# Performance work log

Measured on AMD Instinct MI355X. Metric: run time of the kernel, lower is better.

The kernel has to match this reference:

```python
import jax, jax.numpy as jnp
import numpy as np


def _lrelu(x):
    return jnp.where(x >= 0, x, 0.2 * x)


def _mod_conv(x, style, w_mod, weight, stride, demodulate):
    # x: (B, Cin, H, W); style: (B, S); w_mod: (Cin, S); weight: (Cout, Cin, k, k)
    B, Cin, H, W = x.shape
    Cout, _, k, _ = weight.shape
    scale = 1.0 / np.sqrt(Cin * k * k)
    s = style @ w_mod.T                                   # (B, Cin) per-sample modulation
    w = scale * weight[None] * s[:, None, :, None, None]  # (B, Cout, Cin, k, k)
    if demodulate:
        d = jax.lax.rsqrt(jnp.sum(w * w, axis=(2, 3, 4)) + 1e-8)
        w = w * d[:, :, None, None, None]
    w = w.reshape(B * Cout, Cin, k, k)
    xr = x.reshape(1, B * Cin, H, W)
    pad = k // 2
    out = jax.lax.conv_general_dilated(
        xr, w, (stride, stride), [(pad, pad), (pad, pad)],
        dimension_numbers=('NCHW', 'OIHW', 'NCHW'), feature_group_count=B)
    return out.reshape(B, Cout, out.shape[2], out.shape[3])


def _mapping(z, labels, emb, map_W, map_b, map_g, map_beta):
    x = z + emb[labels]
    for i in range(map_W.shape[0]):
        x = x @ map_W[i].T + map_b[i]
        mu = jnp.mean(x, axis=0)
        var = jnp.var(x, axis=0)  # biased, as torch BatchNorm uses for normalization
        x = (x - mu) * jax.lax.rsqrt(var + 1e-5) * map_g[i] + map_beta[i]
        x = _lrelu(x)
    return x


def _block(x, w, c1w, c1m, c2w, c2m, n1w, n2w, na, nb):
    x = _mod_conv(x, w, c1m, c1w, 1, True)
    x = _lrelu(x + n1w[None, :, None, None] * na)
    x = _mod_conv(x, w, c2m, c2w, 2, True)  # up=2 -> stride=2 strided conv (as in source)
    x = _lrelu(x + n2w[None, :, None, None] * nb)
    return x


def setup_inputs() -> dict:
    key = jax.random.key(0)
    ks = iter(jax.random.split(key, 64))
    nrm = lambda shape, s=1.0: jax.random.normal(next(ks), shape, jnp.float32) * s
    B, Z, Wd, L, LAB = 8, 512, 512, 8, 10
    inp = {}
    inp['z'] = nrm((B, Z))
    inp['labels'] = jax.random.randint(next(ks), (B,), 0, LAB)
    inp['emb'] = nrm((LAB, Z), 0.1)
    inp['map_W'] = nrm((L, Wd, Z), float(np.sqrt(2.0 / Z)))
    inp['map_b'] = jnp.zeros((L, Wd), jnp.float32)
    inp['map_g'] = jnp.ones((L, Wd), jnp.float32)
    inp['map_beta'] = jnp.zeros((L, Wd), jnp.float32)
    inp['const'] = nrm((128, 256, 256))
    inp['b1c1_w'] = nrm((128, 128, 3, 3)); inp['b1c1_m'] = nrm((128, Wd), 0.04)
    inp['b1c2_w'] = nrm((128, 128, 3, 3)); inp['b1c2_m'] = nrm((128, Wd), 0.04)
    inp['b1n1_w'] = nrm((128,), 0.1); inp['b1n2_w'] = nrm((128,), 0.1)
    inp['b2c1_w'] = nrm((64, 128, 3, 3)); inp['b2c1_m'] = nrm((128, Wd), 0.04)
    inp['b2c2_w'] = nrm((64, 64, 3, 3)); inp['b2c2_m'] = nrm((64, Wd), 0.04)
    inp['b2n1_w'] = nrm((64,), 0.1); inp['b2n2_w'] = nrm((64,), 0.1)
    inp['b3c1_w'] = nrm((32, 64, 3, 3)); inp['b3c1_m'] = nrm((64, Wd), 0.04)
    inp['b3c2_w'] = nrm((32, 32, 3, 3)); inp['b3c2_m'] = nrm((32, Wd), 0.04)
    inp['b3n1_w'] = nrm((32,), 0.1); inp['b3n2_w'] = nrm((32,), 0.1)
    inp['rgb_w'] = nrm((1, 32, 1, 1)); inp['rgb_m'] = nrm((32, Wd), 0.04)
    inp['n1a'] = nrm((B, 1, 256, 256)); inp['n1b'] = nrm((B, 1, 128, 128))
    inp['n2a'] = nrm((B, 1, 128, 128)); inp['n2b'] = nrm((B, 1, 64, 64))
    inp['n3a'] = nrm((B, 1, 64, 64)); inp['n3b'] = nrm((B, 1, 32, 32))
    return inp


def reference(z, labels, emb, map_W, map_b, map_g, map_beta, const,
              b1c1_w, b1c1_m, b1c2_w, b1c2_m, b1n1_w, b1n2_w,
              b2c1_w, b2c1_m, b2c2_w, b2c2_m, b2n1_w, b2n2_w,
              b3c1_w, b3c1_m, b3c2_w, b3c2_m, b3n1_w, b3n2_w,
              rgb_w, rgb_m, n1a, n1b, n2a, n2b, n3a, n3b):
    B = z.shape[0]
    w = _mapping(z, labels, emb, map_W, map_b, map_g, map_beta)
    x = jnp.broadcast_to(const[None], (B,) + const.shape)
    x = _block(x, w, b1c1_w, b1c1_m, b1c2_w, b1c2_m, b1n1_w, b1n2_w, n1a, n1b)
    x = _block(x, w, b2c1_w, b2c1_m, b2c2_w, b2c2_m, b2n1_w, b2n2_w, n2a, n2b)
    x = _block(x, w, b3c1_w, b3c1_m, b3c2_w, b3c2_m, b3n1_w, b3n2_w, n3a, n3b)
    # final block: F.interpolate(..., size=(256,240), mode='bilinear', align_corners=False)
    x = jax.image.resize(x, (B, x.shape[1], 256, 240), method='bilinear')
    out = _mod_conv(x, w, rgb_m, rgb_w, 1, False)  # to-grayscale 1x1, no demod
    return out
```

## Files before the change

kernel.cpp:

```cpp
#include <hip/hip_runtime.h>
#include <hip/hip_bf16.h>


typedef __hip_bfloat16 bf16;
typedef __attribute__((ext_vector_type(8))) short bf16x8;
typedef __attribute__((ext_vector_type(4))) float f32x4;

__device__ __forceinline__ float b2f(bf16 v){ return __bfloat162float(v); }
__device__ __forceinline__ bf16  f2b(float v){ return __float2bfloat16(v); }
__device__ __forceinline__ unsigned short bbits(float v){
  bf16 h = f2b(v); union { bf16 h; unsigned short u; } x; x.h = h; return x.u;
}
__device__ __forceinline__ float ldf(const void* p, size_t i, int isf32){
  return isf32 ? ((const float*)p)[i] : b2f(((const bf16*)p)[i]);
}
__device__ __forceinline__ void stf(void* p, size_t i, int isf32, float v){
  if (isf32) ((float*)p)[i] = v; else ((bf16*)p)[i] = f2b(v);
}

__global__ __launch_bounds__(256) void detect_dtype(const unsigned short* __restrict__ cst,
    int* __restrict__ flag){
  __shared__ int cnt[256];
  int t = threadIdx.x, c = 0;
  for (int i=t; i<4096; i+=256){
    unsigned short w = cst[i];
    int mag = w & 0x7FFF;
    int e = mag >> 7;
    if (mag == 0 || (e >= 96 && e <= 150)) c++;
  }
  cnt[t] = c; __syncthreads();
  for (int s=128; s>0; s>>=1){ if (t<s) cnt[t] += cnt[t+s]; __syncthreads(); }
  if (t == 0) *flag = (cnt[0] >= 3500) ? 0 : 1;
}

__global__ __launch_bounds__(256) void cvt_const(const void* __restrict__ cst,
    short* __restrict__ out, const int* __restrict__ dflag){
  int isf32 = *dflag;
  __shared__ __align__(16) short sh[64*136];
  int t = threadIdx.x;
  int p0 = blockIdx.x * 64;
  for (int i=t; i<128*64; i+=256){
    int ci = i >> 6, px = i & 63;
    float v = ldf(cst, (size_t)ci*65536 + p0 + px, isf32);
    sh[px*136 + ci] = (short)bbits(v);
  }
  __syncthreads();
  for (int i=t; i<64*16; i+=256){
    int px = i >> 4, c8 = (i & 15) * 8;
    bf16x8 val = *(const bf16x8*)&sh[px*136 + c8];
    *(bf16x8*)(out + ((size_t)(p0+px))*128 + c8) = val;
  }
}

__global__ __launch_bounds__(256) void map_init(const void* __restrict__ z,
    const int* __restrict__ labels, const void* __restrict__ emb,
    float* __restrict__ x0, const int* __restrict__ dflag){
  int isf32 = *dflag;
  int i = blockIdx.x*256 + threadIdx.x;
  int b = i >> 9, k = i & 511;
  x0[i] = ldf(z, i, isf32) + ldf(emb, (size_t)labels[b]*512 + k, isf32);
}

__global__ __launch_bounds__(64) void map_layer(const float* __restrict__ xin,
    float* __restrict__ xout, const void* __restrict__ W, size_t wOff,
    const void* __restrict__ bl, const void* __restrict__ gl,
    const void* __restrict__ betal, size_t vOff, const int* __restrict__ dflag){
  int isf32 = *dflag;
  int j = blockIdx.x;
  int l = threadIdx.x;
  int b = l >> 3, sp = l & 7;
  float part = 0.f;
  int k0 = sp*64;
  size_t wrow = wOff + (size_t)j*512 + k0;
  for (int k=0; k<64; k++)
    part += xin[b*512 + k0 + k] * ldf(W, wrow + k, isf32);
  part += __shfl_xor(part, 1);
  part += __shfl_xor(part, 2);
  part += __shfl_xor(part, 4);
  float y = part + ldf(bl, vOff + j, isf32);
  float ys[8];
  float mu = 0.f;
  #pragma unroll
  for (int bb=0; bb<8; bb++){ ys[bb] = __shfl(y, bb*8); mu += ys[bb]; }
  mu *= 0.125f;
  float var = 0.f;
  #pragma unroll
  for (int bb=0; bb<8; bb++){ float d = ys[bb]-mu; var += d*d; }
  var *= 0.125f;
  float xn = (y-mu)*rsqrtf(var+1e-5f)*ldf(gl, vOff + j, isf32) + ldf(betal, vOff + j, isf32);
  xn = (xn >= 0.f) ? xn : 0.2f*xn;
  if (sp == 0) xout[b*512 + j] = xn;
}

__global__ __launch_bounds__(64) void styles_kernel(const float* __restrict__ w,
    float* __restrict__ s_all,
    const void* m0, const void* m1, const void* m2, const void* m3,
    const void* m4, const void* m5, const void* m6, const int* __restrict__ dflag){
  int isf32 = *dflag;
  int id = blockIdx.x;
  const int offs[8] = {0,1024,2048,3072,3584,4096,4352,4608};
  const int cins[7] = {128,128,128,64,64,32,32};
  const void* ms[7] = {m0,m1,m2,m3,m4,m5,m6};
  int c = 0;
  while (id >= offs[c+1]) c++;
  int r = id - offs[c];
  int Cin = cins[c];
  int b = r / Cin, ci = r % Cin;
  int l = threadIdx.x;
  float acc = 0.f;
  for (int k=l; k<512; k+=64) acc += w[b*512 + k] * ldf(ms[c], (size_t)ci*512 + k, isf32);
  #pragma unroll
  for (int m=1; m<64; m<<=1) acc += __shfl_xor(acc, m);
  if (l == 0) s_all[id] = acc;
}

__global__ __launch_bounds__(64) void modw_kernel(const float* __restrict__ s_all,
    bf16* __restrict__ wmod,
    const void* w0, const void* w1, const void* w2, const void* w3,
    const void* w4, const void* w5, const void* w6, const int* __restrict__ dflag){
  int isf32 = *dflag;
  int bid = blockIdx.x;
  int base, Cout, Cin, soff, wmoff, demod = 1;
  const void* wp;
  if      (bid < 1024){ base=0;    Cout=128; Cin=128; soff=0;    wmoff=0;       wp=w0; }
  else if (bid < 2048){ base=1024; Cout=128; Cin=128; soff=1024; wmoff=1179648; wp=w1; }
  else if (bid < 2560){ base=2048; Cout=64;  Cin=128; soff=2048; wmoff=2359296; wp=w2; }
  else if (bid < 3072){ base=2560; Cout=64;  Cin=64;  soff=3072; wmoff=2949120; wp=w3; }
  else if (bid < 3328){ base=3072; Cout=32;  Cin=64;  soff=3584; wmoff=3244032; wp=w4; }
  else if (bid < 3584){ base=3328; Cout=32;  Cin=32;  soff=4096; wmoff=3391488; wp=w5; }
  else                { base=3584; Cout=1;   Cin=32;  soff=4352; wmoff=3465216; wp=w6; demod=0; }
  int kk = demod ? 9 : 1;
  int L  = Cin * kk;
  int bc = bid - base;
  int b  = bc / Cout, co = bc % Cout;
  float scale = 1.0f / sqrtf((float)L);
  int l = threadIdx.x;
  float part = 0.f;
  for (int e=l; e<L; e+=64){
    int ci = e / kk;
    float v = scale * ldf(wp, (size_t)co*L + e, isf32) * s_all[soff + b*Cin + ci];
    part += v*v;
  }
  #pragma unroll
  for (int m=1; m<64; m<<=1) part += __shfl_xor(part, m);
  float d = demod ? rsqrtf(part + 1e-8f) : 1.0f;
  for (int e=l; e<L; e+=64){
    int ci = e / kk, tap = e % kk;
    float v = scale * ldf(wp, (size_t)co*L + e, isf32) * s_all[soff + b*Cin + ci];
    size_t idx;
    if (demod){
      int c32 = ci >> 5;
      int lane2 = ((ci >> 3) & 3) * 16 + (co & 15);
      int j = ci & 7;
      int mtg = co >> 4;
      idx = (size_t)wmoff +
            ((((size_t)b*9 + tap)*(Cin>>5) + c32)*(Cout>>4) + mtg)*512 + lane2*8 + j;
    } else {
      idx = (size_t)wmoff + (size_t)b*Cin + e;
    }
    wmod[idx] = f2b(v * d);
  }
}

template<int MT, int NT, int S, int WT, int NR>
__global__ __launch_bounds__(256, 4) void convmf(
    const short* __restrict__ X, long long xbs, int Cin, int Hin, int Win,
    const bf16* __restrict__ WA, const void* __restrict__ noise,
    const void* __restrict__ nwp, short* __restrict__ Y, long long ybs,
    int Cout, int Hout, int Wout, const int* __restrict__ dflag){
  constexpr int W_in_t = (S==1) ? (WT+2) : (2*WT+1);
  constexpr int R_in   = (S==1) ? (NR+2) : (2*NR+1);
  constexpr int ENT    = R_in * W_in_t;
  __shared__ __align__(16) short act[ENT*40];
  int isf32 = *dflag;
  int t = threadIdx.x;
  int lane = t & 63, wv = t >> 6;
  int mw = wv & 1, nwv = wv >> 1;
  int lanelow = lane & 15, quad = lane >> 4;
  int tiles_x = Wout / WT;
  int tx = blockIdx.x % tiles_x, ty = blockIdx.x / tiles_x;
  int ox0 = tx*WT, oy0 = ty*NR;
  int iy0 = S*oy0 - 1, ix0 = S*ox0 - 1;
  int z = blockIdx.z;
  const short* Xb = X + (size_t)z * xbs;
  short* Yb = Y + (size_t)z * ybs;
  const int Cin32 = Cin >> 5, Cout16 = Cout >> 4;
  const bf16x8* WAimg = (const bf16x8*)WA + (size_t)z * 9 * Cin32 * Cout16 * 64;
  f32x4 acc[MT][NT];
  #pragma unroll
  for (int mt=0; mt<MT; mt++)
    #pragma unroll
    for (int nt=0; nt<NT; nt++) acc[mt][nt] = (f32x4){0.f,0.f,0.f,0.f};
  int rowb[NT], xb[NT];
  #pragma unroll
  for (int nt=0; nt<NT; nt++){
    int nl = nwv*NT*16 + nt*16;
    rowb[nt] = nl / WT;
    xb[nt]  = nl % WT + lanelow;
  }
  for (int c32=0; c32<Cin32; c32++){
    int c0 = c32 << 5;
    __syncthreads();
    for (int i=t; i<ENT; i+=256){
      int r = i / W_in_t, x = i - r*W_in_t;
      int gy = iy0 + r, gx = ix0 + x;
      bf16x8* dst = (bf16x8*)&act[i*40];
      if (gy>=0 && gy<Hin && gx>=0 && gx<Win){
        const bf16x8* src = (const bf16x8*)(Xb + ((size_t)gy*Win + gx)*Cin + c0);
        dst[0]=src[0]; dst[1]=src[1]; dst[2]=src[2]; dst[3]=src[3];
      } else {
        bf16x8 zz = (bf16x8){0,0,0,0,0,0,0,0};
        dst[0]=zz; dst[1]=zz; dst[2]=zz; dst[3]=zz;
      }
    }
    __syncthreads();
    #pragma unroll
    for (int tap=0; tap<9; tap++){
      int ky = tap/3, kx = tap%3;
      bf16x8 afr[MT], bfr[NT];
      #pragma unroll
      for (int mt=0; mt<MT; mt++){
        int mtg = mw*MT + mt;
        afr[mt] = WAimg[(((size_t)tap*Cin32 + c32)*Cout16 + mtg)*64 + lane];
      }
      #pragma unroll
      for (int nt=0; nt<NT; nt++){
        int off = ((S*rowb[nt] + ky)*W_in_t + (S*xb[nt] + kx))*40 + quad*8;
        bfr[nt] = *(const bf16x8*)&act[off];
      }
      #pragma unroll
      for (int mt=0; mt<MT; mt++)
        #pragma unroll
        for (int nt=0; nt<NT; nt++)
          acc[mt][nt] = __builtin_amdgcn_mfma_f32_16x16x32_bf16(
              afr[mt], bfr[nt], acc[mt][nt], 0, 0, 0);
    }
  }
  #pragma unroll
  for (int nt=0; nt<NT; nt++){
    int oy = oy0 + rowb[nt], ox = ox0 + xb[nt];
    float nv = ldf(noise, ((size_t)z*Hout + oy)*Wout + ox, isf32);
    #pragma unroll
    for (int mt=0; mt<MT; mt++){
      int co0 = (mw*MT + mt)*16 + quad*4;
      ushort4 pk;
      float v0 = acc[mt][nt][0] + ldf(nwp, co0+0, isf32)*nv; v0 = (v0>=0.f)?v0:0.2f*v0;
      float v1 = acc[mt][nt][1] + ldf(nwp, co0+1, isf32)*nv; v1 = (v1>=0.f)?v1:0.2f*v1;
      float v2 = acc[mt][nt][2] + ldf(nwp, co0+2, isf32)*nv; v2 = (v2>=0.f)?v2:0.2f*v2;
      float v3 = acc[mt][nt][3] + ldf(nwp, co0+3, isf32)*nv; v3 = (v3>=0.f)?v3:0.2f*v3;
      pk.x = bbits(v0); pk.y = bbits(v1); pk.z = bbits(v2); pk.w = bbits(v3);
      *(ushort4*)&Yb[((size_t)oy*Wout + ox)*Cout + co0] = pk;
    }
  }
}

__global__ __launch_bounds__(256) void resize_rgb(const short* __restrict__ X,
    long long xbs, const bf16* __restrict__ wr, void* __restrict__ out,
    const int* __restrict__ dflag){
  int isf32 = *dflag;
  int b = blockIdx.y;
  const short* Xb = X + (size_t)b * xbs;
  int i = blockIdx.x*256 + threadIdx.x;
  int x = i % 240;
  int y = i / 240;
  float sy = (y + 0.5f)*0.125f - 0.5f;
  float sx = (x + 0.5f)*(32.0f/240.0f) - 0.5f;
  float y0f = floorf(sy), x0f = floorf(sx);
  float fy = sy - y0f, fx = sx - x0f;
  int y0 = (int)y0f, x0 = (int)x0f;
  int y1 = min(y0+1, 31), x1 = min(x0+1, 31);
  y0 = max(y0, 0); x0 = max(x0, 0);
  const short* p00 = Xb + ((size_t)(y0*32 + x0))*32;
  const short* p01 = Xb + ((size_t)(y0*32 + x1))*32;
  const short* p10 = Xb + ((size_t)(y1*32 + x0))*32;
  const short* p11 = Xb + ((size_t)(y1*32 + x1))*32;
  float w00 = (1.f-fy)*(1.f-fx), w01 = (1.f-fy)*fx, w10 = fy*(1.f-fx), w11 = fy*fx;
  float acc = 0.f;
  for (int ci=0; ci<32; ci++){
    float v = w00*b2f(((const bf16*)p00)[ci]) + w01*b2f(((const bf16*)p01)[ci])
            + w10*b2f(((const bf16*)p10)[ci]) + w11*b2f(((const bf16*)p11)[ci]);
    acc += b2f(wr[b*32 + ci]) * v;
  }
  stf(out, (size_t)b*61440 + i, isf32, acc);
}

extern "C" void kernel_launch(void* const* d_in, const int* in_sizes, int n_in,
                              void* d_out, int out_size, void* d_ws, size_t ws_size,
                              hipStream_t stream){
  const void* z        = d_in[0];
  const int*  labels   = (const int*)d_in[1];
  const void* emb      = d_in[2];
  const void* map_W    = d_in[3];
  const void* map_b    = d_in[4];
  const void* map_g    = d_in[5];
  const void* map_beta = d_in[6];
  const void* cst      = d_in[7];
  const void* cw0 = d_in[8];   const void* cm0 = d_in[9];
  const void* cw1 = d_in[10];  const void* cm1 = d_in[11];
  const void* n1w = d_in[12];  const void* n2w = d_in[13];
  const void* cw2 = d_in[14];  const void* cm2 = d_in[15];
  const void* cw3 = d_in[16];  const void* cm3 = d_in[17];
  const void* n3w = d_in[18];  const void* n4w = d_in[19];
  const void* cw4 = d_in[20];  const void* cm4 = d_in[21];
  const void* cw5 = d_in[22];  const void* cm5 = d_in[23];
  const void* n5w = d_in[24];  const void* n6w = d_in[25];
  const void* cw6 = d_in[26];  const void* cm6 = d_in[27];
  const void* n1a = d_in[28];  const void* n1b = d_in[29];
  const void* n2a = d_in[30];  const void* n2b = d_in[31];
  const void* n3a = d_in[32];  const void* n3b = d_in[33];

  int*   flag  = (int*)d_ws;
  float* xA    = (float*)((char*)d_ws + 256);
  float* xB    = (float*)((char*)d_ws + 16640);
  float* s_all = (float*)((char*)d_ws + 33024);
  bf16*  wmod  = (bf16*)((char*)d_ws + 51456);
  short* A1    = (short*)((char*)d_ws + 6983680);
  short* A2    = (short*)((char*)d_ws + 141201408);

  detect_dtype<<<1,256,0,stream>>>((const unsigned short*)cst, flag);
  cvt_const<<<1024,256,0,stream>>>(cst, A2, flag);
  map_init<<<16,256,0,stream>>>(z, labels, emb, xA, flag);
  float* cur = xA; float* nxt = xB;
  for (int l=0; l<8; l++){
    map_layer<<<512,64,0,stream>>>(cur, nxt, map_W, (size_t)l*512*512,
                                   map_b, map_g, map_beta, (size_t)l*512, flag);
    float* tmp = cur; cur = nxt; nxt = tmp;
  }
  styles_kernel<<<4608,64,0,stream>>>(cur, s_all, cm0, cm1, cm2, cm3, cm4, cm5, cm6, flag);
  modw_kernel<<<3592,64,0,stream>>>(s_all, wmod, cw0, cw1, cw2, cw3, cw4, cw5, cw6, flag);

  bf16* wm0 = wmod;
  bf16* wm1 = wmod + 1179648;
  bf16* wm2 = wmod + 2359296;
  bf16* wm3 = wmod + 2949120;
  bf16* wm4 = wmod + 3244032;
  bf16* wm5 = wmod + 3391488;
  bf16* wm6 = wmod + 3465216;

  const long long A1e  = 256LL*256*128;
  const long long A1Be = 128LL*128*128;
  const long long A2e  = 128LL*128*64;
  const long long A2Be = 64LL*64*64;
  const long long A3e  = 64LL*64*32;
  const long long A3Be = 32LL*32*32;

  convmf<4,2,1,64,1><<<dim3(1024,1,8),256,0,stream>>>(A2, 0, 128, 256, 256,
      wm0, n1a, n1w, A1, A1e, 128, 256, 256, flag);
  convmf<4,1,2,32,1><<<dim3(512,1,8),256,0,stream>>>(A1, A1e, 128, 256, 256,
      wm1, n1b, n2w, A2, A1Be, 128, 128, 128, flag);
  convmf<2,2,1,64,1><<<dim3(256,1,8),256,0,stream>>>(A2, A1Be, 128, 128, 128,
      wm2, n2a, n3w, A1, A2e, 64, 128, 128, flag);
  convmf<2,1,2,32,1><<<dim3(128,1,8),256,0,stream>>>(A1, A2e, 64, 128, 128,
      wm3, n2b, n4w, A2, A2Be, 64, 64, 64, flag);
  convmf<1,2,1,64,1><<<dim3(64,1,8),256,0,stream>>>(A2, A2Be, 64, 64, 64,
      wm4, n3a, n5w, A1, A3e, 32, 64, 64, flag);
  convmf<1,1,2,32,1><<<dim3(32,1,8),256,0,stream>>>(A1, A3e, 32, 64, 64,
      wm5, n3b, n6w, A2, A3Be, 32, 32, 32, flag);
  resize_rgb<<<dim3(240,8),256,0,stream>>>(A2, A3Be, wm6, d_out, flag);
}
```

Baseline: 709.7 us.

## Switch modulated convs to 32x32x16 MFMA with larger tiles and weight prefetch

Replaces the 16x16x32 bf16 MFMA with 32x32x16 MFMA in the implicit-GEMM conv kernel. The modulated-weight layout is re-packed to match the new operand fragment layout, and per-tap weight fragments are double-buffered so the next tap's weights load while the current tap computes. Pixel tiles are enlarged, and the wave split (MW x NW) becomes a template parameter. The aim is more MACs per instruction and better latency hiding, at the cost of more accumulator registers (launch bounds drop from 4 to 3 blocks per CU) and fewer blocks on the small layers.

```diff
diff --git a/kernel.cpp b/kernel.cpp
--- a/kernel.cpp
+++ b/kernel.cpp
@@ -4,7 +4,7 @@
 
 typedef __hip_bfloat16 bf16;
 typedef __attribute__((ext_vector_type(8))) short bf16x8;
-typedef __attribute__((ext_vector_type(4))) float f32x4;
+typedef __attribute__((ext_vector_type(16))) float f32x16;
 
 __device__ __forceinline__ float b2f(bf16 v){ return __bfloat162float(v); }
 __device__ __forceinline__ bf16  f2b(float v){ return __float2bfloat16(v); }
@@ -150,11 +150,13 @@
     size_t idx;
     if (demod){
       int c32 = ci >> 5;
-      int lane2 = ((ci >> 3) & 3) * 16 + (co & 15);
+      int cog = co >> 5;
+      int kt  = (ci >> 4) & 1;
+      int lane2 = ((ci >> 3) & 1)*32 + (co & 31);
       int j = ci & 7;
-      int mtg = co >> 4;
       idx = (size_t)wmoff +
-            ((((size_t)b*9 + tap)*(Cin>>5) + c32)*(Cout>>4) + mtg)*512 + lane2*8 + j;
+            ((((size_t)b*9 + tap)*(Cin>>5) + c32)*(Cout>>5) + cog)*1024 +
+            kt*512 + lane2*8 + j;
     } else {
       idx = (size_t)wmoff + (size_t)b*Cin + e;
     }
@@ -162,12 +164,14 @@
   }
 }
 
-template<int MT, int NT, int S, int WT, int NR>
-__global__ __launch_bounds__(256, 4) void convmf(
+template<int MT2, int NT2, int MW, int NW, int S, int WT, int NR>
+__global__ __launch_bounds__(256, 3) void convmf(
     const short* __restrict__ X, long long xbs, int Cin, int Hin, int Win,
     const bf16* __restrict__ WA, const void* __restrict__ noise,
     const void* __restrict__ nwp, short* __restrict__ Y, long long ybs,
     int Cout, int Hout, int Wout, const int* __restrict__ dflag){
+  static_assert(MW*NW == 4, "4 waves");
+  static_assert(NW*NT2*32 == WT*NR, "pixel tile");
   constexpr int W_in_t = (S==1) ? (WT+2) : (2*WT+1);
   constexpr int R_in   = (S==1) ? (NR+2) : (2*NR+1);
   constexpr int ENT    = R_in * W_in_t;
@@ -175,8 +179,8 @@
   int isf32 = *dflag;
   int t = threadIdx.x;
   int lane = t & 63, wv = t >> 6;
-  int mw = wv & 1, nwv = wv >> 1;
-  int lanelow = lane & 15, quad = lane >> 4;
+  int mw = wv % MW, nwv = wv / MW;
+  int lane32 = lane & 31, half = lane >> 5;
   int tiles_x = Wout / WT;
   int tx = blockIdx.x % tiles_x, ty = blockIdx.x / tiles_x;
   int ox0 = tx*WT, oy0 = ty*NR;
@@ -184,20 +188,23 @@
   int z = blockIdx.z;
   const short* Xb = X + (size_t)z * xbs;
   short* Yb = Y + (size_t)z * ybs;
-  const int Cin32 = Cin >> 5, Cout16 = Cout >> 4;
-  const bf16x8* WAimg = (const bf16x8*)WA + (size_t)z * 9 * Cin32 * Cout16 * 64;
-  f32x4 acc[MT][NT];
-  #pragma unroll
-  for (int mt=0; mt<MT; mt++)
+  const int Cin32 = Cin >> 5, Cout32 = Cout >> 5;
+  const bf16x8* WAimg = (const bf16x8*)WA + (size_t)z * 9 * Cin32 * Cout32 * 128;
+  f32x16 acc[MT2][NT2];
+  #pragma unroll
+  for (int mt=0; mt<MT2; mt++)
     #pragma unroll
-    for (int nt=0; nt<NT; nt++) acc[mt][nt] = (f32x4){0.f,0.f,0.f,0.f};
-  int rowb[NT], xb[NT];
-  #pragma unroll
-  for (int nt=0; nt<NT; nt++){
-    int nl = nwv*NT*16 + nt*16;
+    for (int nt=0; nt<NT2; nt++)
+      #pragma unroll
+      for (int e=0; e<16; e++) acc[mt][nt][e] = 0.f;
+  int rowb[NT2], xb[NT2];
+  #pragma unroll
+  for (int nt=0; nt<NT2; nt++){
+    int nl = (nwv*NT2 + nt)*32;
     rowb[nt] = nl / WT;
-    xb[nt]  = nl % WT + lanelow;
-  }
+    xb[nt]  = nl % WT + lane32;
+  }
+  bf16x8 afr[2][MT2][2];
   for (int c32=0; c32<Cin32; c32++){
     int c0 = c32 << 5;
     __syncthreads();
@@ -214,42 +221,61 @@
       }
     }
     __syncthreads();
+    const bf16x8* WAc = WAimg + (size_t)c32 * Cout32 * 128;
+    #pragma unroll
+    for (int mt=0; mt<MT2; mt++)
+      #pragma unroll
+      for (int kt=0; kt<2; kt++)
+        afr[0][mt][kt] = WAc[((size_t)(mw*MT2+mt))*128 + kt*64 + lane];
     #pragma unroll
     for (int tap=0; tap<9; tap++){
+      constexpr int dummy = 0; (void)dummy;
+      int cur = tap & 1, nxt = cur ^ 1;
+      if (tap < 8){
+        #pragma unroll
+        for (int mt=0; mt<MT2; mt++)
+          #pragma unroll
+          for (int kt=0; kt<2; kt++)
+            afr[nxt][mt][kt] = WAc[(size_t)(tap+1)*Cin32*Cout32*128 +
+                                   ((size_t)(mw*MT2+mt))*128 + kt*64 + lane];
+      }
       int ky = tap/3, kx = tap%3;
-      bf16x8 afr[MT], bfr[NT];
-      #pragma unroll
-      for (int mt=0; mt<MT; mt++){
-        int mtg = mw*MT + mt;
-        afr[mt] = WAimg[(((size_t)tap*Cin32 + c32)*Cout16 + mtg)*64 + lane];
+      bf16x8 bfr[NT2][2];
+      #pragma unroll
+      for (int nt=0; nt<NT2; nt++){
+        int entry = (S*rowb[nt] + ky)*W_in_t + (S*xb[nt] + kx);
+        #pragma unroll
+        for (int kt=0; kt<2; kt++)
+          bfr[nt][kt] = *(const bf16x8*)&act[entry*40 + kt*16 + half*8];
       }
       #pragma unroll
-      for (int nt=0; nt<NT; nt++){
-        int off = ((S*rowb[nt] + ky)*W_in_t + (S*xb[nt] + kx))*40 + quad*8;
-        bfr[nt] = *(const bf16x8*)&act[off];
-      }
-      #pragma unroll
-      for (int mt=0; mt<MT; mt++)
+      for (int mt=0; mt<MT2; mt++)
         #pragma unroll
-        for (int nt=0; nt<NT; nt++)
-          acc[mt][nt] = __builtin_amdgcn_mfma_f32_16x16x32_bf16(
-              afr[mt], bfr[nt], acc[mt][nt], 0, 0, 0);
+        for (int nt=0; nt<NT2; nt++)
+          #pragma unroll
+          for (int kt=0; kt<2; kt++)
+            acc[mt][nt] = __builtin_amdgcn_mfma_f32_32x32x16_bf16(
+                afr[cur][mt][kt], bfr[nt][kt], acc[mt][nt], 0, 0, 0);
     }
   }
   #pragma unroll
-  for (int nt=0; nt<NT; nt++){
+  for (int nt=0; nt<NT2; nt++){
     int oy = oy0 + rowb[nt], ox = ox0 + xb[nt];
     float nv = ldf(noise, ((size_t)z*Hout + oy)*Wout + ox, isf32);
     #pragma unroll
-    for (int mt=0; mt<MT; mt++){
-      int co0 = (mw*MT + mt)*16 + quad*4;
-      ushort4 pk;
-      float v0 = acc[mt][nt][0] + ldf(nwp, co0+0, isf32)*nv; v0 = (v0>=0.f)?v0:0.2f*v0;
-      float v1 = acc[mt][nt][1] + ldf(nwp, co0+1, isf32)*nv; v1 = (v1>=0.f)?v1:0.2f*v1;
-      float v2 = acc[mt][nt][2] + ldf(nwp, co0+2, isf32)*nv; v2 = (v2>=0.f)?v2:0.2f*v2;
-      float v3 = acc[mt][nt][3] + ldf(nwp, co0+3, isf32)*nv; v3 = (v3>=0.f)?v3:0.2f*v3;
-      pk.x = bbits(v0); pk.y = bbits(v1); pk.z = bbits(v2); pk.w = bbits(v3);
-      *(ushort4*)&Yb[((size_t)oy*Wout + ox)*Cout + co0] = pk;
+    for (int mt=0; mt<MT2; mt++){
+      int cobase = (mw*MT2 + mt)*32 + half*4;
+      #pragma unroll
+      for (int g=0; g<4; g++){
+        int co0 = cobase + 8*g;
+        ushort4 pk;
+        float v0 = acc[mt][nt][4*g+0] + ldf(nwp, co0+0, isf32)*nv; v0=(v0>=0.f)?v0:0.2f*v0;
+        float v1 = acc[mt][nt][4*g+1] + ldf(nwp, co0+1, isf32)*nv; v1=(v1>=0.f)?v1:0.2f*v1;
+        float v2 = acc[mt][nt][4*g+2] + ldf(nwp, co0+2, isf32)*nv; v2=(v2>=0.f)?v2:0.2f*v2;
+        float v3 = acc[mt][nt][4*g+3] + ldf(nwp, co0+3, isf32)*nv; v3=(v3>=0.f)?v3:0.2f*v3;
+        pk.x = bbits(v0); pk.y = bbits(v1); pk.z = bbits(v2); pk.w = bbits(v3);
+        *(ushort4*)&Yb[((size_t)oy*Wout + ox)*Cout + co0] = pk;
+      }
     }
   }
 }
@@ -344,17 +370,17 @@
   const long long A3e  = 64LL*64*32;
   const long long A3Be = 32LL*32*32;
 
-  convmf<4,2,1,64,1><<<dim3(1024,1,8),256,0,stream>>>(A2, 0, 128, 256, 256,
+  convmf<2,2,2,2,1,128,1><<<dim3(512,1,8),256,0,stream>>>(A2, 0, 128, 256, 256,
       wm0, n1a, n1w, A1, A1e, 128, 256, 256, flag);
-  convmf<4,1,2,32,1><<<dim3(512,1,8),256,0,stream>>>(A1, A1e, 128, 256, 256,
+  convmf<2,1,2,2,2,64,1><<<dim3(256,1,8),256,0,stream>>>(A1, A1e, 128, 256, 256,
       wm1, n1b, n2w, A2, A1Be, 128, 128, 128, flag);
-  convmf<2,2,1,64,1><<<dim3(256,1,8),256,0,stream>>>(A2, A1Be, 128, 128, 128,
+  convmf<1,2,2,2,1,128,1><<<dim3(128,1,8),256,0,stream>>>(A2, A1Be, 128, 128, 128,
       wm2, n2a, n3w, A1, A2e, 64, 128, 128, flag);
-  convmf<2,1,2,32,1><<<dim3(128,1,8),256,0,stream>>>(A1, A2e, 64, 128, 128,
+  convmf<1,1,2,2,2,64,1><<<dim3(64,1,8),256,0,stream>>>(A1, A2e, 64, 128, 128,
       wm3, n2b, n4w, A2, A2Be, 64, 64, 64, flag);
-  convmf<1,2,1,64,1><<<dim3(64,1,8),256,0,stream>>>(A2, A2Be, 64, 64, 64,
+  convmf<1,2,1,4,1,64,4><<<dim3(16,1,8),256,0,stream>>>(A2, A2Be, 64, 64, 64,
       wm4, n3a, n5w, A1, A3e, 32, 64, 64, flag);
-  convmf<1,1,2,32,1><<<dim3(32,1,8),256,0,stream>>>(A1, A3e, 32, 64, 64,
+  convmf<1,1,1,4,2,32,4><<<dim3(8,1,8),256,0,stream>>>(A1, A3e, 32, 64, 64,
       wm5, n3b, n6w, A2, A3Be, 32, 32, 32, flag);
   resize_rgb<<<dim3(240,8),256,0,stream>>>(A2, A3Be, wm6, d_out, flag);
 }
```

New measurement: 659.3 us. 7.1% less time.
